# Performance work log

Hardware: AMD Instinct MI355X
Metric: run time of the kernel (lower is better)

Reference implementation:

```python
import jax, jax.numpy as jnp
import numpy as np

N = 50000      # nodes
R = 3          # relations
E = 600000     # edges per relation
D_IN, D_HID, D_OUT = 128, 256, 128


def setup_inputs() -> dict:
    key = jax.random.key(0)
    ks = jax.random.split(key, 9)
    s = 0.05  # weight scale
    x = jax.random.normal(ks[0], (N, D_IN), jnp.float32)
    src = jax.random.randint(ks[1], (R, E), 0, N, dtype=jnp.int32)
    dst = jax.random.randint(ks[2], (R, E), 0, N, dtype=jnp.int32)
    Wself1 = jax.random.normal(ks[3], (R, D_IN, D_HID), jnp.float32) * s
    Wneigh1 = jax.random.normal(ks[4], (R, D_IN, D_HID), jnp.float32) * s
    b1 = jnp.zeros((R, D_HID), jnp.float32)
    Wself2 = jax.random.normal(ks[5], (R, D_HID, D_OUT), jnp.float32) * s
    Wneigh2 = jax.random.normal(ks[6], (R, D_HID, D_OUT), jnp.float32) * s
    b2 = jnp.zeros((R, D_OUT), jnp.float32)
    return dict(x=x, src=src, dst=dst, Wself1=Wself1, Wneigh1=Wneigh1, b1=b1,
                Wself2=Wself2, Wneigh2=Wneigh2, b2=b2)


def _hetero_sage_layer(x, src, dst, Wself, Wneigh, b):
    """Sum over relations of SAGEConv(mean): fc_self(x) + fc_neigh(mean_agg(x)) + b."""
    def mean_agg(s, d):
        seg = jax.ops.segment_sum(x[s], d, num_segments=N)                # [N, d]
        deg = jax.ops.segment_sum(jnp.ones((s.shape[0],), x.dtype), d,
                                  num_segments=N)                         # [N]
        return seg / jnp.maximum(deg, 1.0)[:, None]                       # 0-indeg nodes -> 0

    mean = jax.vmap(mean_agg)(src, dst)                                   # [R, N, d_in]
    # sum_r (x @ Wself_r) = x @ sum_r Wself_r  (HeteroGraphConv aggregate='sum')
    return (x @ Wself.sum(0)
            + jnp.einsum('rnd,rdh->nh', mean, Wneigh)
            + b.sum(0))


def reference(x, src, dst, Wself1, Wneigh1, b1, Wself2, Wneigh2, b2):
    h = jax.nn.relu(_hetero_sage_layer(x, src, dst, Wself1, Wneigh1, b1))
    return _hetero_sage_layer(h, src, dst, Wself2, Wneigh2, b2)
```

## Files before the change

kernel.cpp:

```cpp
#include <hip/hip_runtime.h>
#include <hip/hip_bf16.h>
#include <cstddef>


#define NN 50000
#define RR 3
#define EE 600000
#define DIN 128
#define DHID 256
#define DOUT 128
#define NRN (RR * NN)

#define RANGE 256
#define NRANGE ((NN + RANGE - 1) / RANGE)
#define NBIN (RR * NRANGE)
#define EPB 4096
#define NBLK ((RR * EE + EPB - 1) / EPB)
#define MAXB2 4096
#define MTOT (NBIN * NBLK)

typedef __hip_bfloat16 bf16;
typedef __hip_bfloat162 bf162;
typedef unsigned short u16;
typedef __attribute__((ext_vector_type(8))) short short8;
typedef __attribute__((ext_vector_type(4))) float floatx4;

__device__ __forceinline__ void async_copy16(const void* g, void* l) {
    __builtin_amdgcn_global_load_lds((const __attribute__((address_space(1))) void*)g,
                                     (__attribute__((address_space(3))) void*)l, 16, 0, 0);
}

#define PREP_A (NN * 64)
#define PREP_B (256 * 512)
#define PREP_C (512 * 256)
#define PREP_D 384
#define PREP_TOTAL (PREP_A + PREP_B + PREP_C + PREP_D)
#define PREP_BLOCKS ((PREP_TOTAL + 255) / 256)

__global__ __launch_bounds__(256) void hist_prep(const int* __restrict__ dst,
        int* __restrict__ m,
        const float* __restrict__ x,
        const float* __restrict__ Ws1, const float* __restrict__ Wn1,
        const float* __restrict__ b1,
        const float* __restrict__ Ws2, const float* __restrict__ Wn2,
        const float* __restrict__ b2,
        bf16* __restrict__ Abig, bf16* __restrict__ B1t, bf16* __restrict__ B2t,
        float* __restrict__ bias1, float* __restrict__ bias2) {
    __shared__ int lh[NBIN];
    if (blockIdx.x < NBLK) {
        for (int i = threadIdx.x; i < NBIN; i += 256) lh[i] = 0;
        __syncthreads();
        int base = blockIdx.x * EPB;
        int lim = min(EPB, RR * EE - base);
        for (int i = threadIdx.x; i < lim; i += 256) {
            int e = base + i;
            int r = e / EE;
            int d = dst[e];
            atomicAdd(&lh[r * NRANGE + (d >> 8)], 1);
        }
        __syncthreads();
        for (int i = threadIdx.x; i < NBIN; i += 256) m[i * NBLK + blockIdx.x] = lh[i];
        return;
    }
    int idx = (blockIdx.x - NBLK) * 256 + threadIdx.x;
    if (idx < PREP_A) {
        int n = idx >> 6, c2 = idx & 63;
        float2 v = *(const float2*)&x[(size_t)n * DIN + c2 * 2];
        bf162 o; o.x = __float2bfloat16(v.x); o.y = __float2bfloat16(v.y);
        *(bf162*)&Abig[(size_t)n * 512 + c2 * 2] = o;
        return;
    }
    idx -= PREP_A;
    if (idx < PREP_B) {
        int n = idx >> 9, k = idx & 511;
        float v;
        if (k < 128) {
            v = Ws1[(size_t)k * 256 + n]
              + Ws1[(size_t)(128 + k) * 256 + n]
              + Ws1[(size_t)(256 + k) * 256 + n];
        } else {
            int q = k - 128; int r = q >> 7; int kk = q & 127;
            v = Wn1[((size_t)r * 128 + kk) * 256 + n];
        }
        B1t[(size_t)n * 512 + k] = __float2bfloat16(v);
        return;
    }
    idx -= PREP_B;
    if (idx < PREP_C) {
        int n = idx >> 8, k = idx & 255;
        float v;
        if (n < 128) {
            v = Ws2[(size_t)k * 128 + n]
              + Ws2[(size_t)(256 + k) * 128 + n]
              + Ws2[(size_t)(512 + k) * 128 + n];
        } else {
            int q = n - 128; int r = q >> 7; int nn = q & 127;
            v = Wn2[((size_t)r * 256 + k) * 128 + nn];
        }
        B2t[(size_t)n * 256 + k] = __float2bfloat16(v);
        return;
    }
    idx -= PREP_C;
    if (idx < PREP_D) {
        if (idx < 256) {
            bias1[idx] = b1[idx] + b1[256 + idx] + b1[512 + idx];
        } else {
            int j = idx - 256;
            bias2[j] = b2[j] + b2[128 + j] + b2[256 + j];
        }
    }
}

__global__ __launch_bounds__(256) void mscan_blocks(int* __restrict__ data,
        int* __restrict__ bsums, int n) {
    int t = threadIdx.x;
    int base = blockIdx.x * 1024 + t * 4;
    int v[4];
    #pragma unroll
    for (int i = 0; i < 4; ++i) v[i] = (base + i < n) ? data[base + i] : 0;
    int s = v[0] + v[1] + v[2] + v[3];
    int lane = t & 63, wid = t >> 6;
    int sc = s;
    #pragma unroll
    for (int d = 1; d < 64; d <<= 1) {
        int tt = __shfl_up(sc, d, 64);
        if (lane >= d) sc += tt;
    }
    __shared__ int wsum[4], woff[4];
    if (lane == 63) wsum[wid] = sc;
    __syncthreads();
    if (t == 0) {
        int a = 0;
        #pragma unroll
        for (int i = 0; i < 4; ++i) { woff[i] = a; a += wsum[i]; }
    }
    __syncthreads();
    int run = sc - s + woff[wid];
    #pragma unroll
    for (int i = 0; i < 4; ++i) {
        if (base + i < n) data[base + i] = run;
        run += v[i];
    }
    if (t == 255) bsums[blockIdx.x] = woff[3] + wsum[3];
}

__global__ __launch_bounds__(256) void mscan_sums(int* __restrict__ bsums, int nb) {
    int t = threadIdx.x;
    int v = (t < nb) ? bsums[t] : 0;
    int lane = t & 63, wid = t >> 6;
    int sc = v;
    #pragma unroll
    for (int d = 1; d < 64; d <<= 1) {
        int tt = __shfl_up(sc, d, 64);
        if (lane >= d) sc += tt;
    }
    __shared__ int wsum[4], woff[4];
    if (lane == 63) wsum[wid] = sc;
    __syncthreads();
    if (t == 0) {
        int a = 0;
        #pragma unroll
        for (int i = 0; i < 4; ++i) { woff[i] = a; a += wsum[i]; }
    }
    __syncthreads();
    if (t < nb) bsums[t] = sc - v + woff[wid];
}

__global__ __launch_bounds__(256) void mscan_fixup(int* __restrict__ m,
        const int* __restrict__ bsums, int* __restrict__ binbase) {
    int i = blockIdx.x * 256 + threadIdx.x;
    if (i < MTOT) {
        int v = m[i] + bsums[i >> 10];
        m[i] = v;
        int q = i / NBLK;
        if (i - q * NBLK == 0) binbase[q] = v;
    }
    if (i == 0) binbase[NBIN] = RR * EE;
}

__global__ __launch_bounds__(256) void binscatter(const int* __restrict__ src,
        const int* __restrict__ dst, const int* __restrict__ m,
        unsigned* __restrict__ ebuf) {
    __shared__ int scur[NBIN];
    for (int i = threadIdx.x; i < NBIN; i += 256) scur[i] = m[i * NBLK + blockIdx.x];
    __syncthreads();
    int base = blockIdx.x * EPB;
    int lim = min(EPB, RR * EE - base);
    for (int i = threadIdx.x; i < lim; i += 256) {
        int e = base + i;
        int r = e / EE;
        int d = dst[e];
        int pos = atomicAdd(&scur[r * NRANGE + (d >> 8)], 1);
        ebuf[pos] = ((unsigned)(d & 255) << 16) | (unsigned)src[e];
    }
}

__global__ __launch_bounds__(256) void binsort(const int* __restrict__ binbase,
        const unsigned* __restrict__ ebuf, u16* __restrict__ col,
        int* __restrict__ rowptr) {
    int b = blockIdx.x;
    int r = b / NRANGE, rb = b - r * NRANGE;
    int node0 = rb * RANGE;
    int nn = min(RANGE, NN - node0);
    int beg = binbase[b], end = binbase[b + 1];
    int cnt = min(end - beg, MAXB2);

    __shared__ unsigned eb[MAXB2];
    __shared__ u16 sb[MAXB2];
    __shared__ int lh[RANGE], lc[RANGE];
    __shared__ int wsum[4], woff[4];

    for (int i = threadIdx.x; i < cnt; i += 256) eb[i] = ebuf[beg + i];
    lh[threadIdx.x] = 0;
    __syncthreads();
    for (int i = threadIdx.x; i < cnt; i += 256) atomicAdd(&lh[eb[i] >> 16], 1);
    __syncthreads();
    {
        int t = threadIdx.x, lane = t & 63, wid = t >> 6;
        int v = lh[t];
        int sc = v;
        #pragma unroll
        for (int d = 1; d < 64; d <<= 1) {
            int tt = __shfl_up(sc, d, 64);
            if (lane >= d) sc += tt;
        }
        if (lane == 63) wsum[wid] = sc;
        __syncthreads();
        if (t == 0) {
            int a = 0;
            #pragma unroll
            for (int i = 0; i < 4; ++i) { woff[i] = a; a += wsum[i]; }
        }
        __syncthreads();
        int excl = sc - v + woff[wid];
        lc[t] = excl;
        if (t < nn) rowptr[r * NN + node0 + t] = beg + excl;
        if (t == 0) rowptr[r * NN + node0 + nn] = end;
    }
    __syncthreads();
    for (int i = threadIdx.x; i < cnt; i += 256) {
        unsigned e = eb[i];
        int pos = atomicAdd(&lc[e >> 16], 1);
        sb[pos] = (u16)(e & 0xffffu);
    }
    __syncthreads();
    for (int i = threadIdx.x; i < cnt; i += 256) col[beg + i] = sb[i];
}

__device__ __forceinline__ float bflo(unsigned u) { return __uint_as_float(u << 16); }
__device__ __forceinline__ float bfhi(unsigned u) { return __uint_as_float(u & 0xffff0000u); }

__global__ __launch_bounds__(256) void gather1(const int* __restrict__ rowptr,
        const u16* __restrict__ col, bf16* __restrict__ Abig) {
    int g = blockIdx.x * 4 + (threadIdx.x >> 6);
    int lane = threadIdx.x & 63;
    int r = g / NN;
    int n = g - r * NN;
    int beg = rowptr[g], end = rowptr[g + 1];
    const unsigned* xb = (const unsigned*)Abig;
    float acc0 = 0.f, acc1 = 0.f;
    for (int base = beg; base < end; base += 64) {
        int cnt = min(64, end - base);
        int cidx = (lane < cnt) ? (int)col[base + lane] : 0;
        int j = 0;
        for (; j + 8 <= cnt; j += 8) {
            const unsigned* p0 = xb + (size_t)__builtin_amdgcn_readlane(cidx, j)     * 256;
            const unsigned* p1 = xb + (size_t)__builtin_amdgcn_readlane(cidx, j + 1) * 256;
            const unsigned* p2 = xb + (size_t)__builtin_amdgcn_readlane(cidx, j + 2) * 256;
            const unsigned* p3 = xb + (size_t)__builtin_amdgcn_readlane(cidx, j + 3) * 256;
            const unsigned* p4 = xb + (size_t)__builtin_amdgcn_readlane(cidx, j + 4) * 256;
            const unsigned* p5 = xb + (size_t)__builtin_amdgcn_readlane(cidx, j + 5) * 256;
            const unsigned* p6 = xb + (size_t)__builtin_amdgcn_readlane(cidx, j + 6) * 256;
            const unsigned* p7 = xb + (size_t)__builtin_amdgcn_readlane(cidx, j + 7) * 256;
            unsigned u0 = p0[lane], u1 = p1[lane], u2 = p2[lane], u3 = p3[lane];
            unsigned u4 = p4[lane], u5 = p5[lane], u6 = p6[lane], u7 = p7[lane];
            acc0 += bflo(u0) + bflo(u1) + bflo(u2) + bflo(u3)
                  + bflo(u4) + bflo(u5) + bflo(u6) + bflo(u7);
            acc1 += bfhi(u0) + bfhi(u1) + bfhi(u2) + bfhi(u3)
                  + bfhi(u4) + bfhi(u5) + bfhi(u6) + bfhi(u7);
        }
        for (; j + 4 <= cnt; j += 4) {
            const unsigned* p0 = xb + (size_t)__builtin_amdgcn_readlane(cidx, j)     * 256;
            const unsigned* p1 = xb + (size_t)__builtin_amdgcn_readlane(cidx, j + 1) * 256;
            const unsigned* p2 = xb + (size_t)__builtin_amdgcn_readlane(cidx, j + 2) * 256;
            const unsigned* p3 = xb + (size_t)__builtin_amdgcn_readlane(cidx, j + 3) * 256;
            unsigned u0 = p0[lane], u1 = p1[lane], u2 = p2[lane], u3 = p3[lane];
            acc0 += bflo(u0) + bflo(u1) + bflo(u2) + bflo(u3);
            acc1 += bfhi(u0) + bfhi(u1) + bfhi(u2) + bfhi(u3);
        }
        for (; j < cnt; ++j) {
            const unsigned* p = xb + (size_t)__builtin_amdgcn_readlane(cidx, j) * 256;
            unsigned u = p[lane];
            acc0 += bflo(u);
            acc1 += bfhi(u);
        }
    }
    float inv = 1.0f / fmaxf((float)(end - beg), 1.0f);
    bf162 o;
    o.x = __float2bfloat16(acc0 * inv);
    o.y = __float2bfloat16(acc1 * inv);
    *(bf162*)&Abig[(size_t)n * 512 + 128 + r * 128 + lane * 2] = o;
}

__global__ __launch_bounds__(256) void gemm12(bf16* AY,
        const bf16* __restrict__ B1t, const bf16* __restrict__ B2t,
        const float* __restrict__ bias1, const float* __restrict__ bias2,
        float* __restrict__ out) {
    __shared__ bf16 hT[128 * 264];
    __shared__ short As[128 * 32];
    const int t = threadIdx.x;
    const int wv = t >> 6, lane = t & 63;
    const int wr = wv >> 1, wc = wv & 1;
    const int m16 = lane & 15, kg = lane >> 4;
    const int s = blockIdx.x;
    const int row0 = s * 128;
    const int ldrow = t >> 2, ldk = (t & 3) * 8;
    const int arow0 = min(row0 + ldrow, NN - 1);
    const int arow1 = min(row0 + ldrow + 64, NN - 1);
    const short* Ag0 = (const short*)AY + (size_t)arow0 * 512 + ldk;
    const short* Ag1 = (const short*)AY + (size_t)arow1 * 512 + ldk;
    short* AsW = &As[(size_t)wv * 512];
    const short* B1s = (const short*)B1t;
    const short* B2s = (const short*)B2t;

    floatx4 acc1[2][4][4] = {};
    for (int kb = 0; kb < 512; kb += 32) {
        async_copy16(Ag0 + kb, AsW);
        async_copy16(Ag1 + kb, AsW + 2048);
        __syncthreads();
        short8 a[4];
        #pragma unroll
        for (int i = 0; i < 4; ++i)
            a[i] = *(const short8*)&As[(wr * 64 + i * 16 + m16) * 32 + kg * 8];
        #pragma unroll
        for (int ch = 0; ch < 2; ++ch) {
            short8 b[4];
            #pragma unroll
            for (int j = 0; j < 4; ++j)
                b[j] = *(const short8*)&B1s[(size_t)(ch * 128 + wc * 64 + j * 16 + m16) * 512 + kb + kg * 8];
            #pragma unroll
            for (int i = 0; i < 4; ++i)
                #pragma unroll
                for (int j = 0; j < 4; ++j)
                    acc1[ch][i][j] = __builtin_amdgcn_mfma_f32_16x16x32_bf16(a[i], b[j], acc1[ch][i][j], 0, 0, 0);
        }
        __syncthreads();
    }
    #pragma unroll
    for (int ch = 0; ch < 2; ++ch)
        #pragma unroll
        for (int j = 0; j < 4; ++j) {
            int c = ch * 128 + wc * 64 + j * 16 + m16;
            float bj = bias1[c];
            #pragma unroll
            for (int i = 0; i < 4; ++i) {
                int rl = wr * 64 + i * 16 + kg * 4;
                #pragma unroll
                for (int reg = 0; reg < 4; ++reg)
                    hT[(rl + reg) * 264 + c] =
                        __float2bfloat16(fmaxf(acc1[ch][i][j][reg] + bj, 0.f));
            }
        }
    __syncthreads();

    #pragma unroll 1
    for (int ct = 0; ct < 4; ++ct) {
        floatx4 acc[4][4] = {};
        for (int kb = 0; kb < 256; kb += 32) {
            short8 a[4], b[4];
            #pragma unroll
            for (int i = 0; i < 4; ++i)
                a[i] = *(const short8*)&((const short*)hT)[(wr * 64 + i * 16 + m16) * 264 + kb + kg * 8];
            #pragma unroll
            for (int j = 0; j < 4; ++j)
                b[j] = *(const short8*)&B2s[(size_t)(ct * 128 + wc * 64 + j * 16 + m16) * 256 + kb + kg * 8];
            #pragma unroll
            for (int i = 0; i < 4; ++i)
                #pragma unroll
                for (int j = 0; j < 4; ++j)
                    acc[i][j] = __builtin_amdgcn_mfma_f32_16x16x32_bf16(a[i], b[j], acc[i][j], 0, 0, 0);
        }
        if (ct == 0) {
            #pragma unroll
            for (int j = 0; j < 4; ++j) {
                int c = wc * 64 + j * 16 + m16;
                float bj = bias2[c];
                #pragma unroll
                for (int i = 0; i < 4; ++i) {
                    int rl = wr * 64 + i * 16 + kg * 4;
                    #pragma unroll
                    for (int reg = 0; reg < 4; ++reg) {
                        int r = row0 + rl + reg;
                        if (r < NN) out[(size_t)r * DOUT + c] = acc[i][j][reg] + bj;
                    }
                }
            }
        } else {
            int rel = ct - 1;
            bf16* yp = AY + ((size_t)s << 16) + ((size_t)rel << 14);
            #pragma unroll
            for (int j = 0; j < 4; ++j) {
                int c = wc * 64 + j * 16 + m16;
                #pragma unroll
                for (int i = 0; i < 4; ++i) {
                    int rl = wr * 64 + i * 16 + kg * 4;
                    #pragma unroll
                    for (int reg = 0; reg < 4; ++reg) {
                        if (row0 + rl + reg < NN)
                            yp[((rl + reg) << 7) + c] = __float2bfloat16(acc[i][j][reg]);
                    }
                }
            }
        }
        __syncthreads();
    }
}

__global__ __launch_bounds__(256) void gather2(const bf16* __restrict__ ypack,
        const int* __restrict__ rowptr, const u16* __restrict__ col,
        float* __restrict__ out) {
    int n = blockIdx.x * 4 + (threadIdx.x >> 6);
    int lane = threadIdx.x & 63;
    float2 acc = *(float2*)&out[(size_t)n * DOUT + lane * 2];
    const unsigned* yb = (const unsigned*)ypack;
    #pragma unroll
    for (int r = 0; r < RR; ++r) {
        int g = r * NN + n;
        int beg = rowptr[g], end = rowptr[g + 1];
        float a0 = 0.f, a1 = 0.f;
        const size_t rbase = (size_t)r << 13;
        for (int base = beg; base < end; base += 64) {
            int cnt = min(64, end - base);
            int cidx = (lane < cnt) ? (int)col[base + lane] : 0;
            int j = 0;
            for (; j + 8 <= cnt; j += 8) {
                int s0 = __builtin_amdgcn_readlane(cidx, j);
                int s1 = __builtin_amdgcn_readlane(cidx, j + 1);
                int s2 = __builtin_amdgcn_readlane(cidx, j + 2);
                int s3 = __builtin_amdgcn_readlane(cidx, j + 3);
                int s4 = __builtin_amdgcn_readlane(cidx, j + 4);
                int s5 = __builtin_amdgcn_readlane(cidx, j + 5);
                int s6 = __builtin_amdgcn_readlane(cidx, j + 6);
                int s7 = __builtin_amdgcn_readlane(cidx, j + 7);
                const unsigned* p0 = yb + rbase + ((size_t)(s0 >> 7) << 15) + ((s0 & 127) << 6);
                const unsigned* p1 = yb + rbase + ((size_t)(s1 >> 7) << 15) + ((s1 & 127) << 6);
                const unsigned* p2 = yb + rbase + ((size_t)(s2 >> 7) << 15) + ((s2 & 127) << 6);
                const unsigned* p3 = yb + rbase + ((size_t)(s3 >> 7) << 15) + ((s3 & 127) << 6);
                const unsigned* p4 = yb + rbase + ((size_t)(s4 >> 7) << 15) + ((s4 & 127) << 6);
                const unsigned* p5 = yb + rbase + ((size_t)(s5 >> 7) << 15) + ((s5 & 127) << 6);
                const unsigned* p6 = yb + rbase + ((size_t)(s6 >> 7) << 15) + ((s6 & 127) << 6);
                const unsigned* p7 = yb + rbase + ((size_t)(s7 >> 7) << 15) + ((s7 & 127) << 6);
                unsigned u0 = p0[lane], u1 = p1[lane], u2 = p2[lane], u3 = p3[lane];
                unsigned u4 = p4[lane], u5 = p5[lane], u6 = p6[lane], u7 = p7[lane];
                a0 += bflo(u0) + bflo(u1) + bflo(u2) + bflo(u3)
                    + bflo(u4) + bflo(u5) + bflo(u6) + bflo(u7);
                a1 += bfhi(u0) + bfhi(u1) + bfhi(u2) + bfhi(u3)
                    + bfhi(u4) + bfhi(u5) + bfhi(u6) + bfhi(u7);
            }
            for (; j < cnt; ++j) {
                int sj = __builtin_amdgcn_readlane(cidx, j);
                const unsigned* p = yb + rbase + ((size_t)(sj >> 7) << 15) + ((sj & 127) << 6);
                unsigned u = p[lane];
                a0 += bflo(u);
                a1 += bfhi(u);
            }
        }
        float inv = 1.0f / fmaxf((float)(end - beg), 1.0f);
        acc.x += a0 * inv;
        acc.y += a1 * inv;
    }
    *(float2*)&out[(size_t)n * DOUT + lane * 2] = acc;
}

extern "C" void kernel_launch(void* const* d_in, const int* in_sizes, int n_in,
                              void* d_out, int out_size, void* d_ws, size_t ws_size,
                              hipStream_t stream) {
    const float* x       = (const float*)d_in[0];
    const int*   src     = (const int*)  d_in[1];
    const int*   dst     = (const int*)  d_in[2];
    const float* Wself1  = (const float*)d_in[3];
    const float* Wneigh1 = (const float*)d_in[4];
    const float* b1      = (const float*)d_in[5];
    const float* Wself2  = (const float*)d_in[6];
    const float* Wneigh2 = (const float*)d_in[7];
    const float* b2      = (const float*)d_in[8];
    float* out = (float*)d_out;

    char* ws = (char*)d_ws;
    int*      mtx     = (int*)     (ws + 0x0000000ull);
    int*      binbase = (int*)     (ws + 0x0110000ull);
    int*      bsums   = (int*)     (ws + 0x0120000ull);
    int*      rowptr  = (int*)     (ws + 0x0140000ull);
    float*    bias1   = (float*)   (ws + 0x01E1000ull);
    float*    bias2   = (float*)   (ws + 0x01E2000ull);
    unsigned* ebuf    = (unsigned*)(ws + 0x0200000ull);
    bf16*     B1t     = (bf16*)    (ws + 0x0A00000ull);
    bf16*     B2t     = (bf16*)    (ws + 0x0A40000ull);
    bf16*     Abig    = (bf16*)    (ws + 0x0B00000ull);
    u16*      col     = (u16*)     (ws + 0x5600000ull);

    hist_prep<<<NBLK + PREP_BLOCKS, 256, 0, stream>>>(
        dst, mtx, x, Wself1, Wneigh1, b1, Wself2, Wneigh2, b2,
        Abig, B1t, B2t, bias1, bias2);

    mscan_blocks<<<(MTOT + 1023) / 1024, 256, 0, stream>>>(mtx, bsums, MTOT);
    mscan_sums<<<1, 256, 0, stream>>>(bsums, (MTOT + 1023) / 1024);
    mscan_fixup<<<(MTOT + 255) / 256, 256, 0, stream>>>(mtx, bsums, binbase);
    binscatter<<<NBLK, 256, 0, stream>>>(src, dst, mtx, ebuf);
    binsort<<<NBIN, 256, 0, stream>>>(binbase, ebuf, col, rowptr);

    gather1<<<NRN / 4, 256, 0, stream>>>(rowptr, col, Abig);

    gemm12<<<(NN + 127) / 128, 256, 0, stream>>>(Abig, B1t, B2t, bias1, bias2, out);

    gather2<<<NN / 4, 256, 0, stream>>>(Abig, rowptr, col, out);
}
```

Before: 385.3 us.

## Shrink fused GEMM row tile to 64 with XOR-swizzled LDS for hidden activations

```diff
diff --git a/kernel.cpp b/kernel.cpp
--- a/kernel.cpp
+++ b/kernel.cpp
@@ -306,88 +306,85 @@
         const bf16* __restrict__ B1t, const bf16* __restrict__ B2t,
         const float* __restrict__ bias1, const float* __restrict__ bias2,
         float* __restrict__ out) {
-    __shared__ bf16 hT[128 * 264];
-    __shared__ short As[128 * 32];
+    __shared__ bf16 hT[64 * 256];
+    __shared__ short As[64 * 32];
+    char* hTb = (char*)hT;
     const int t = threadIdx.x;
-    const int wv = t >> 6, lane = t & 63;
-    const int wr = wv >> 1, wc = wv & 1;
+    const int w = t >> 6, lane = t & 63;
     const int m16 = lane & 15, kg = lane >> 4;
     const int s = blockIdx.x;
-    const int row0 = s * 128;
+    const int row0 = s * 64;
     const int ldrow = t >> 2, ldk = (t & 3) * 8;
-    const int arow0 = min(row0 + ldrow, NN - 1);
-    const int arow1 = min(row0 + ldrow + 64, NN - 1);
-    const short* Ag0 = (const short*)AY + (size_t)arow0 * 512 + ldk;
-    const short* Ag1 = (const short*)AY + (size_t)arow1 * 512 + ldk;
-    short* AsW = &As[(size_t)wv * 512];
+    const int arow = min(row0 + ldrow, NN - 1);
+    const short* Ag = (const short*)AY + (size_t)arow * 512 + ldk;
+    short* AsW = &As[(size_t)w * 512];
     const short* B1s = (const short*)B1t;
     const short* B2s = (const short*)B2t;
 
-    floatx4 acc1[2][4][4] = {};
+    floatx4 acc1[4][4] = {};
     for (int kb = 0; kb < 512; kb += 32) {
-        async_copy16(Ag0 + kb, AsW);
-        async_copy16(Ag1 + kb, AsW + 2048);
+        async_copy16(Ag + kb, AsW);
         __syncthreads();
         short8 a[4];
         #pragma unroll
         for (int i = 0; i < 4; ++i)
-            a[i] = *(const short8*)&As[(wr * 64 + i * 16 + m16) * 32 + kg * 8];
-        #pragma unroll
-        for (int ch = 0; ch < 2; ++ch) {
-            short8 b[4];
+            a[i] = *(const short8*)&As[(i * 16 + m16) * 32 + kg * 8];
+        short8 b[4];
+        #pragma unroll
+        for (int j = 0; j < 4; ++j)
+            b[j] = *(const short8*)&B1s[(size_t)(w * 64 + j * 16 + m16) * 512 + kb + kg * 8];
+        #pragma unroll
+        for (int i = 0; i < 4; ++i)
             #pragma unroll
             for (int j = 0; j < 4; ++j)
-                b[j] = *(const short8*)&B1s[(size_t)(ch * 128 + wc * 64 + j * 16 + m16) * 512 + kb + kg * 8];
+                acc1[i][j] = __builtin_amdgcn_mfma_f32_16x16x32_bf16(a[i], b[j], acc1[i][j], 0, 0, 0);
+        __syncthreads();
+    }
+    #pragma unroll
+    for (int j = 0; j < 4; ++j) {
+        int c = w * 64 + j * 16 + m16;
+        float bj = bias1[c];
+        #pragma unroll
+        for (int i = 0; i < 4; ++i) {
+            int rl = i * 16 + kg * 4;
+            #pragma unroll
+            for (int reg = 0; reg < 4; ++reg) {
+                int rr = rl + reg;
+                int off = ((rr * 256 + c) * 2) ^ ((rr & 7) << 4);
+                *(bf16*)(hTb + off) = __float2bfloat16(fmaxf(acc1[i][j][reg] + bj, 0.f));
+            }
+        }
+    }
+    __syncthreads();
+
+    #pragma unroll 1
+    for (int ct = 0; ct < 4; ++ct) {
+        floatx4 acc[4][2] = {};
+        for (int kb = 0; kb < 256; kb += 32) {
+            short8 a[4], b[2];
+            #pragma unroll
+            for (int i = 0; i < 4; ++i) {
+                int rr = i * 16 + m16;
+                int off = ((rr * 256 + kb + kg * 8) * 2) ^ ((rr & 7) << 4);
+                a[i] = *(const short8*)(hTb + off);
+            }
+            #pragma unroll
+            for (int j = 0; j < 2; ++j)
+                b[j] = *(const short8*)&B2s[(size_t)(ct * 128 + w * 32 + j * 16 + m16) * 256 + kb + kg * 8];
             #pragma unroll
             for (int i = 0; i < 4; ++i)
                 #pragma unroll
-                for (int j = 0; j < 4; ++j)
-                    acc1[ch][i][j] = __builtin_amdgcn_mfma_f32_16x16x32_bf16(a[i], b[j], acc1[ch][i][j], 0, 0, 0);
-        }
-        __syncthreads();
-    }
-    #pragma unroll
-    for (int ch = 0; ch < 2; ++ch)
-        #pragma unroll
-        for (int j = 0; j < 4; ++j) {
-            int c = ch * 128 + wc * 64 + j * 16 + m16;
-            float bj = bias1[c];
-            #pragma unroll
-            for (int i = 0; i < 4; ++i) {
-                int rl = wr * 64 + i * 16 + kg * 4;
-                #pragma unroll
-                for (int reg = 0; reg < 4; ++reg)
-                    hT[(rl + reg) * 264 + c] =
-                        __float2bfloat16(fmaxf(acc1[ch][i][j][reg] + bj, 0.f));
-            }
-        }
-    __syncthreads();
-
-    #pragma unroll 1
-    for (int ct = 0; ct < 4; ++ct) {
-        floatx4 acc[4][4] = {};
-        for (int kb = 0; kb < 256; kb += 32) {
-            short8 a[4], b[4];
-            #pragma unroll
-            for (int i = 0; i < 4; ++i)
-                a[i] = *(const short8*)&((const short*)hT)[(wr * 64 + i * 16 + m16) * 264 + kb + kg * 8];
-            #pragma unroll
-            for (int j = 0; j < 4; ++j)
-                b[j] = *(const short8*)&B2s[(size_t)(ct * 128 + wc * 64 + j * 16 + m16) * 256 + kb + kg * 8];
-            #pragma unroll
-            for (int i = 0; i < 4; ++i)
-                #pragma unroll
-                for (int j = 0; j < 4; ++j)
+                for (int j = 0; j < 2; ++j)
                     acc[i][j] = __builtin_amdgcn_mfma_f32_16x16x32_bf16(a[i], b[j], acc[i][j], 0, 0, 0);
         }
         if (ct == 0) {
             #pragma unroll
-            for (int j = 0; j < 4; ++j) {
-                int c = wc * 64 + j * 16 + m16;
+            for (int j = 0; j < 2; ++j) {
+                int c = w * 32 + j * 16 + m16;
                 float bj = bias2[c];
                 #pragma unroll
                 for (int i = 0; i < 4; ++i) {
-                    int rl = wr * 64 + i * 16 + kg * 4;
+                    int rl = i * 16 + kg * 4;
                     #pragma unroll
                     for (int reg = 0; reg < 4; ++reg) {
                         int r = row0 + rl + reg;
@@ -397,13 +394,13 @@
             }
         } else {
             int rel = ct - 1;
-            bf16* yp = AY + ((size_t)s << 16) + ((size_t)rel << 14);
-            #pragma unroll
-            for (int j = 0; j < 4; ++j) {
-                int c = wc * 64 + j * 16 + m16;
+            bf16* yp = AY + ((size_t)s << 15) + ((size_t)rel << 13);
+            #pragma unroll
+            for (int j = 0; j < 2; ++j) {
+                int c = w * 32 + j * 16 + m16;
                 #pragma unroll
                 for (int i = 0; i < 4; ++i) {
-                    int rl = wr * 64 + i * 16 + kg * 4;
+                    int rl = i * 16 + kg * 4;
                     #pragma unroll
                     for (int reg = 0; reg < 4; ++reg) {
                         if (row0 + rl + reg < NN)
@@ -412,7 +409,6 @@
                 }
             }
         }
-        __syncthreads();
     }
 }
 
@@ -428,7 +424,7 @@
         int g = r * NN + n;
         int beg = rowptr[g], end = rowptr[g + 1];
         float a0 = 0.f, a1 = 0.f;
-        const size_t rbase = (size_t)r << 13;
+        const size_t rbase = (size_t)r << 12;
         for (int base = beg; base < end; base += 64) {
             int cnt = min(64, end - base);
             int cidx = (lane < cnt) ? (int)col[base + lane] : 0;
@@ -442,14 +438,14 @@
                 int s5 = __builtin_amdgcn_readlane(cidx, j + 5);
                 int s6 = __builtin_amdgcn_readlane(cidx, j + 6);
                 int s7 = __builtin_amdgcn_readlane(cidx, j + 7);
-                const unsigned* p0 = yb + rbase + ((size_t)(s0 >> 7) << 15) + ((s0 & 127) << 6);
-                const unsigned* p1 = yb + rbase + ((size_t)(s1 >> 7) << 15) + ((s1 & 127) << 6);
-                const unsigned* p2 = yb + rbase + ((size_t)(s2 >> 7) << 15) + ((s2 & 127) << 6);
-                const unsigned* p3 = yb + rbase + ((size_t)(s3 >> 7) << 15) + ((s3 & 127) << 6);
-                const unsigned* p4 = yb + rbase + ((size_t)(s4 >> 7) << 15) + ((s4 & 127) << 6);
-                const unsigned* p5 = yb + rbase + ((size_t)(s5 >> 7) << 15) + ((s5 & 127) << 6);
-                const unsigned* p6 = yb + rbase + ((size_t)(s6 >> 7) << 15) + ((s6 & 127) << 6);
-                const unsigned* p7 = yb + rbase + ((size_t)(s7 >> 7) << 15) + ((s7 & 127) << 6);
+                const unsigned* p0 = yb + rbase + ((size_t)(s0 >> 6) << 14) + ((s0 & 63) << 6);
+                const unsigned* p1 = yb + rbase + ((size_t)(s1 >> 6) << 14) + ((s1 & 63) << 6);
+                const unsigned* p2 = yb + rbase + ((size_t)(s2 >> 6) << 14) + ((s2 & 63) << 6);
+                const unsigned* p3 = yb + rbase + ((size_t)(s3 >> 6) << 14) + ((s3 & 63) << 6);
+                const unsigned* p4 = yb + rbase + ((size_t)(s4 >> 6) << 14) + ((s4 & 63) << 6);
+                const unsigned* p5 = yb + rbase + ((size_t)(s5 >> 6) << 14) + ((s5 & 63) << 6);
+                const unsigned* p6 = yb + rbase + ((size_t)(s6 >> 6) << 14) + ((s6 & 63) << 6);
+                const unsigned* p7 = yb + rbase + ((size_t)(s7 >> 6) << 14) + ((s7 & 63) << 6);
                 unsigned u0 = p0[lane], u1 = p1[lane], u2 = p2[lane], u3 = p3[lane];
                 unsigned u4 = p4[lane], u5 = p5[lane], u6 = p6[lane], u7 = p7[lane];
                 a0 += bflo(u0) + bflo(u1) + bflo(u2) + bflo(u3)
@@ -459,7 +455,7 @@
             }
             for (; j < cnt; ++j) {
                 int sj = __builtin_amdgcn_readlane(cidx, j);
-                const unsigned* p = yb + rbase + ((size_t)(sj >> 7) << 15) + ((sj & 127) << 6);
+                const unsigned* p = yb + rbase + ((size_t)(sj >> 6) << 14) + ((sj & 63) << 6);
                 unsigned u = p[lane];
                 a0 += bflo(u);
                 a1 += bfhi(u);
@@ -511,7 +507,7 @@
 
     gather1<<<NRN / 4, 256, 0, stream>>>(rowptr, col, Abig);
 
-    gemm12<<<(NN + 127) / 128, 256, 0, stream>>>(Abig, B1t, B2t, bias1, bias2, out);
+    gemm12<<<(NN + 63) / 64, 256, 0, stream>>>(Abig, B1t, B2t, bias1, bias2, out);
 
     gather2<<<NN / 4, 256, 0, stream>>>(Abig, rowptr, col, out);
 }
```

Measured after the change: 401.6 us. 4.2% more time.
